# Kernel tuning notes

Measured on AMD Instinct MI355X. Metric: run time of the kernel, lower is better.

Reference implementation:

```python
import jax, jax.numpy as jnp
import numpy as np
import math

B, L, H, D = 4, 2048, 8, 64
FACTOR = 5
SAMPLE_K = min(FACTOR * int(np.ceil(np.log(L))), L)  # U_part = 40
N_TOP = min(FACTOR * int(np.ceil(np.log(L))), L)     # u = 40


def setup_inputs() -> dict:
    key = jax.random.key(0)
    kq, kk, kv, ki = jax.random.split(key, 4)
    queries = jax.random.normal(kq, (B, L, H, D), dtype=jnp.float32)
    keys = jax.random.normal(kk, (B, L, H, D), dtype=jnp.float32)
    values = jax.random.normal(kv, (B, L, H, D), dtype=jnp.float32)
    # ProbSparse random key sampling indices (torch.randint(L_K, (L_Q, sample_k)))
    index_sample = jax.random.randint(ki, (L, SAMPLE_K), 0, L, dtype=jnp.int64)
    return {"queries": queries, "keys": keys, "values": values,
            "index_sample": index_sample}


def reference(queries, keys, values, index_sample):
    # [B, L, H, D] -> [B, H, L, D]
    Q = jnp.transpose(queries, (0, 2, 1, 3))
    K = jnp.transpose(keys, (0, 2, 1, 3))
    V = jnp.transpose(values, (0, 2, 1, 3))
    L_K = K.shape[2]

    # --- _prob_QK ---
    # gather sampled keys per query: [B, H, L_Q, sample_k, D]
    K_sample = K[:, :, index_sample, :]
    # sampled QK dots: [B, H, L_Q, sample_k]
    Q_K_sample = jnp.einsum('bhld,bhlsd->bhls', Q, K_sample)
    # sparsity measurement M = max - mean
    M = Q_K_sample.max(axis=-1) - Q_K_sample.sum(axis=-1) / L_K  # [B, H, L_Q]
    _, M_top = jax.lax.top_k(M, N_TOP)  # [B, H, n_top]
    # gather top queries: [B, H, n_top, D]
    Q_reduce = jnp.take_along_axis(Q, M_top[..., None], axis=2)
    # reduced scores against all keys: [B, H, n_top, L_K]
    scores_top = jnp.einsum('bhud,bhkd->bhuk', Q_reduce, K)

    # --- forward tail ---
    scale = 1.0 / math.sqrt(D)
    attn = jax.nn.softmax(scores_top * scale, axis=-1)  # dropout = identity (eval)
    context = jnp.einsum('bhuk,bhkd->bhud', attn, V)  # [B, H, n_top, D]
    # [B, n_top, H, D]
    return jnp.transpose(context, (0, 2, 1, 3))
```

## Files before the change

### kernel.cpp

```cpp
#include <hip/hip_runtime.h>
#include <hip/hip_bf16.h>

#define BB 4
#define LL 2048
#define HH 8
#define DD 64
#define SK 40
#define NT 40
#define CH 256
#define NCH (LL / CH)
#define QH 20

#define WS 10

typedef float f4 __attribute__((ext_vector_type(4)));

__global__ __launch_bounds__(256, 6) void compute_m_kernel(
        const float* __restrict__ Q, const float* __restrict__ K,
        const int* __restrict__ idx, float* __restrict__ M) {
    __shared__ float2 mlpart[4][HH];

    int blk = blockIdx.x;
    int x = blk & 7, g = blk >> 3;
    int b = x >> 1;
    int l = (g << 1) | (x & 1);
    int t = threadIdx.x;
    int lane = t & 63, w = t >> 6;
    int grp  = lane >> 3;

    const float* Qrow = Q + ((size_t)b * LL + l) * 512 + lane * 8;
    f4 qa = *(const f4*)(Qrow);
    f4 qb = *(const f4*)(Qrow + 4);

    const float* Kb = K + (size_t)b * LL * 512 + lane * 8;
    const int* ib = idx + (size_t)l * SK + w * WS;

    int i0 = ib[0], i1 = ib[1], i2 = ib[2], i3 = ib[3], i4 = ib[4];
    int i5 = ib[5], i6 = ib[6], i7 = ib[7], i8 = ib[8], i9 = ib[9];
    const float* a0 = Kb + (size_t)i0 * 512;
    const float* a1 = Kb + (size_t)i1 * 512;
    const float* a2 = Kb + (size_t)i2 * 512;
    const float* a3 = Kb + (size_t)i3 * 512;
    const float* a4 = Kb + (size_t)i4 * 512;
    const float* a5 = Kb + (size_t)i5 * 512;
    const float* a6 = Kb + (size_t)i6 * 512;
    const float* a7 = Kb + (size_t)i7 * 512;
    const float* a8 = Kb + (size_t)i8 * 512;
    const float* a9 = Kb + (size_t)i9 * 512;

    asm volatile("" : "+v"(qa), "+v"(qb));

    f4 A0, B0, A1, B1, A2, B2, A3, B3, A4, B4;
    f4 A5, B5, A6, B6, A7, B7, A8, B8, A9, B9;

    #define ISSUE(AV, BV, PTR)                                                  \
        asm volatile("global_load_dwordx4 %0, %2, off\n"                        \
                     "global_load_dwordx4 %1, %2, off offset:16"                \
                     : "=&v"(AV), "=&v"(BV) : "v"(PTR))

    float mx = -INFINITY, sm = 0.0f;

    #define CONS(AV, BV, WAIT) do {                                            \
        asm volatile(WAIT : "+v"(AV), "+v"(BV));                               \
        float p = qa.x*AV.x + qa.y*AV.y + qa.z*AV.z + qa.w*AV.w                \
                + qb.x*BV.x + qb.y*BV.y + qb.z*BV.z + qb.w*BV.w;               \
        p += __shfl_xor(p, 1, 64);                                             \
        p += __shfl_xor(p, 2, 64);                                             \
        p += __shfl_xor(p, 4, 64);                                             \
        mx = fmaxf(mx, p);                                                     \
        sm += p;                                                               \
    } while (0)

    ISSUE(A0, B0, a0); ISSUE(A1, B1, a1); ISSUE(A2, B2, a2);
    ISSUE(A3, B3, a3); ISSUE(A4, B4, a4);
    ISSUE(A5, B5, a5); CONS(A0, B0, "s_waitcnt vmcnt(10)");
    ISSUE(A6, B6, a6); CONS(A1, B1, "s_waitcnt vmcnt(10)");
    ISSUE(A7, B7, a7); CONS(A2, B2, "s_waitcnt vmcnt(10)");
    ISSUE(A8, B8, a8); CONS(A3, B3, "s_waitcnt vmcnt(10)");
    ISSUE(A9, B9, a9); CONS(A4, B4, "s_waitcnt vmcnt(10)");
    CONS(A5, B5, "s_waitcnt vmcnt(8)");
    CONS(A6, B6, "s_waitcnt vmcnt(6)");
    CONS(A7, B7, "s_waitcnt vmcnt(4)");
    CONS(A8, B8, "s_waitcnt vmcnt(2)");
    CONS(A9, B9, "s_waitcnt vmcnt(0)");
    #undef ISSUE
    #undef CONS

    if ((lane & 7) == 0)
        mlpart[w][grp] = make_float2(mx, sm);
    __syncthreads();

    if (t < HH) {
        float MX = -INFINITY, SM = 0.0f;
        #pragma unroll
        for (int w2 = 0; w2 < 4; ++w2) {
            float2 ml = mlpart[w2][t];
            MX = fmaxf(MX, ml.x);
            SM += ml.y;
        }
        M[((size_t)b * HH + t) * LL + l] = MX - SM * (1.0f / (float)LL);
    }
}

__global__ __launch_bounds__(256) void topk_kernel(const float* __restrict__ M,
                                                   int* __restrict__ topi) {
    __shared__ unsigned long long keys[LL];
    __shared__ unsigned long long wmax[4];
    __shared__ int win;
    int bh = blockIdx.x;
    int t  = threadIdx.x;
    int lane = t & 63, w = t >> 6;

    unsigned long long kmax = 0ULL;
    #pragma unroll
    for (int j = 0; j < 8; ++j) {
        int i = t + 256 * j;
        unsigned int bits = __float_as_uint(M[(size_t)bh * LL + i]);
        bits = (bits & 0x80000000u) ? ~bits : (bits | 0x80000000u);
        unsigned long long k = ((unsigned long long)bits << 11)
                             | (unsigned int)(LL - 1 - i);
        keys[i] = k;
        if (k > kmax) kmax = k;
    }
    __syncthreads();

    for (int u = 0; u < NT; ++u) {
        unsigned long long k = kmax;
        #pragma unroll
        for (int off = 32; off >= 1; off >>= 1) {
            unsigned long long o = __shfl_xor(k, off, 64);
            if (o > k) k = o;
        }
        if (lane == 0) wmax[w] = k;
        __syncthreads();
        if (t == 0) {
            unsigned long long k0 = wmax[0];
            if (wmax[1] > k0) k0 = wmax[1];
            if (wmax[2] > k0) k0 = wmax[2];
            if (wmax[3] > k0) k0 = wmax[3];
            int i = (LL - 1) - (int)(k0 & 0x7FF);
            topi[bh * NT + u] = i;
            keys[i] = 0ULL;
            win = i;
        }
        __syncthreads();
        if ((win & 255) == t) {
            kmax = 0ULL;
            #pragma unroll
            for (int j = 0; j < 8; ++j) {
                unsigned long long kk = keys[t + 256 * j];
                if (kk > kmax) kmax = kk;
            }
        }
    }
}

__global__ __launch_bounds__(256, 3) void attn_kernel(
        const float* __restrict__ Q, const float* __restrict__ K,
        const float* __restrict__ V, const int* __restrict__ topi,
        float2* __restrict__ pml, float* __restrict__ po) {
    __shared__ float  qs[QH][DD];
    __shared__ float4 e4buf[4][64];
    __shared__ float  oarea[4][QH][DD];
    __shared__ float  mlarea[4][QH][2];

    int blk = blockIdx.x;
    int qh  = blk >> 8;
    int cc2 = blk & 255;
    int c   = cc2 & (NCH - 1);
    int bh  = cc2 >> 3;
    int h = bh & (HH - 1), b = bh >> 3;
    int t = threadIdx.x, lane = t & 63, w = t >> 6;
    int u0 = qh * QH;

    for (int i = t; i < QH * DD; i += 256) {
        int u = i >> 6, d = i & 63;
        int lq = topi[bh * NT + u0 + u];
        qs[u][d] = Q[(((size_t)b * LL + lq) * HH + h) * DD + d];
    }

    int key = c * CH + w * 64 + lane;
    const float4* kr = (const float4*)&K[(((size_t)b * LL + key) * HH + h) * DD];
    float4 kreg[16];
    #pragma unroll
    for (int j = 0; j < 16; ++j) kreg[j] = kr[j];

    float vcol[64];
    const float* vb = &V[(((size_t)b * LL + c * CH + w * 64) * HH + h) * DD + lane];
    #pragma unroll
    for (int j = 0; j < 64; ++j) vcol[j] = vb[(size_t)j * HH * DD];

    __syncthreads();

    for (int uq = 0; uq < QH / 4; ++uq) {
        float o0 = 0, o1 = 0, o2 = 0, o3 = 0;
        float mv0, mv1, mv2, mv3, lv0, lv1, lv2, lv3;
        float4 ev;
        #pragma unroll
        for (int j = 0; j < 4; ++j) {
            int u = uq * 4 + j;
            const float4* q4 = (const float4*)&qs[u][0];
            float s = 0.0f;
            #pragma unroll
            for (int cc = 0; cc < 16; ++cc) {
                float4 qv = q4[cc];
                s += qv.x * kreg[cc].x + qv.y * kreg[cc].y
                   + qv.z * kreg[cc].z + qv.w * kreg[cc].w;
            }
            s *= 0.125f;
            float m = s;
            #pragma unroll
            for (int off = 32; off >= 1; off >>= 1)
                m = fmaxf(m, __shfl_xor(m, off, 64));
            float e = __expf(s - m);
            float ls = e;
            #pragma unroll
            for (int off = 32; off >= 1; off >>= 1)
                ls += __shfl_xor(ls, off, 64);
            if (j == 0) { mv0 = m; lv0 = ls; ev.x = e; }
            if (j == 1) { mv1 = m; lv1 = ls; ev.y = e; }
            if (j == 2) { mv2 = m; lv2 = ls; ev.z = e; }
            if (j == 3) { mv3 = m; lv3 = ls; ev.w = e; }
        }
        e4buf[w][lane] = ev;
        asm volatile("s_waitcnt lgkmcnt(0)" ::: "memory");
        #pragma unroll
        for (int l2 = 0; l2 < 64; ++l2) {
            float4 e = e4buf[w][l2];
            float  v = vcol[l2];
            o0 += e.x * v; o1 += e.y * v; o2 += e.z * v; o3 += e.w * v;
        }
        oarea[w][uq * 4 + 0][lane] = o0;
        oarea[w][uq * 4 + 1][lane] = o1;
        oarea[w][uq * 4 + 2][lane] = o2;
        oarea[w][uq * 4 + 3][lane] = o3;
        if (lane == 0) {
            mlarea[w][uq * 4 + 0][0] = mv0; mlarea[w][uq * 4 + 0][1] = lv0;
            mlarea[w][uq * 4 + 1][0] = mv1; mlarea[w][uq * 4 + 1][1] = lv1;
            mlarea[w][uq * 4 + 2][0] = mv2; mlarea[w][uq * 4 + 2][1] = lv2;
            mlarea[w][uq * 4 + 3][0] = mv3; mlarea[w][uq * 4 + 3][1] = lv3;
        }
    }
    __syncthreads();

    for (int i = t; i < QH * DD; i += 256) {
        int u = i >> 6, d = i & 63;
        float m0 = mlarea[0][u][0], m1 = mlarea[1][u][0];
        float m2 = mlarea[2][u][0], m3 = mlarea[3][u][0];
        float mb = fmaxf(fmaxf(m0, m1), fmaxf(m2, m3));
        float s0 = __expf(m0 - mb), s1 = __expf(m1 - mb);
        float s2 = __expf(m2 - mb), s3 = __expf(m3 - mb);
        float ob = oarea[0][u][d] * s0 + oarea[1][u][d] * s1
                 + oarea[2][u][d] * s2 + oarea[3][u][d] * s3;
        int gu = u0 + u;
        po[((size_t)(bh * NT + gu) * NCH + c) * DD + d] = ob;
        if (d == 0) {
            float lb = mlarea[0][u][1] * s0 + mlarea[1][u][1] * s1
                     + mlarea[2][u][1] * s2 + mlarea[3][u][1] * s3;
            pml[(bh * NT + gu) * NCH + c] = make_float2(mb, lb);
        }
    }
}

__global__ __launch_bounds__(256) void merge_kernel(
        const float2* __restrict__ pml, const float* __restrict__ po,
        float* __restrict__ out) {
    int wid  = blockIdx.x * 4 + (threadIdx.x >> 6);
    int lane = threadIdx.x & 63;
    int u  = wid % NT;
    int bh = wid / NT;
    int h = bh & (HH - 1), b = bh >> 3;
    int base = (bh * NT + u) * NCH;

    float m = -INFINITY;
    #pragma unroll
    for (int cc = 0; cc < NCH; ++cc) m = fmaxf(m, pml[base + cc].x);
    float lsum = 0.0f, o = 0.0f;
    #pragma unroll
    for (int cc = 0; cc < NCH; ++cc) {
        float2 ml = pml[base + cc];
        float sc = __expf(ml.x - m);
        lsum += ml.y * sc;
        o    += po[(size_t)(base + cc) * DD + lane] * sc;
    }
    out[(((size_t)b * NT + u) * HH + h) * DD + lane] = o / lsum;
}

extern "C" void kernel_launch(void* const* d_in, const int* in_sizes, int n_in,
                              void* d_out, int out_size, void* d_ws, size_t ws_size,
                              hipStream_t stream) {
    const float* Q   = (const float*)d_in[0];
    const float* K   = (const float*)d_in[1];
    const float* V   = (const float*)d_in[2];
    const int*   idx = (const int*)d_in[3];
    float* out = (float*)d_out;

    char* ws = (char*)d_ws;
    float*  M    = (float*)ws;                        ws += (size_t)BB * HH * LL * sizeof(float);
    int*    topi = (int*)ws;                          ws += (size_t)BB * HH * NT * sizeof(int);
    float2* pml  = (float2*)ws;                       ws += (size_t)BB * HH * NT * NCH * sizeof(float2);
    float*  po   = (float*)ws;

    hipLaunchKernelGGL(compute_m_kernel, dim3(BB * LL), dim3(256), 0, stream,
                       Q, K, idx, M);
    hipLaunchKernelGGL(topk_kernel, dim3(BB * HH), dim3(256), 0, stream, M, topi);
    hipLaunchKernelGGL(attn_kernel, dim3(2 * BB * HH * NCH), dim3(256), 0, stream,
                       Q, K, V, topi, pml, po);
    hipLaunchKernelGGL(merge_kernel, dim3(BB * HH * NT / 4), dim3(256), 0, stream,
                       pml, po, out);
}
```

Measured before the change: 166.6 us.

## Restructure top-k as per-wave register top-40 then single-wave merge

The top-k selection now keeps each wave's 512 keys in registers and has each wave independently extract its local top-40 by repeated wave-wide shuffle max, with no block barriers inside the loop. The 160 candidates are then merged by one wave into the global top-40. This removes the two __syncthreads per iteration and the 2048-entry shared key array, at the cost of more register pressure and redundant per-wave work.

```diff
diff --git a/kernel.cpp b/kernel.cpp
--- a/kernel.cpp
+++ b/kernel.cpp
@@ -104,53 +104,54 @@
 
 __global__ __launch_bounds__(256) void topk_kernel(const float* __restrict__ M,
                                                    int* __restrict__ topi) {
-    __shared__ unsigned long long keys[LL];
-    __shared__ unsigned long long wmax[4];
-    __shared__ int win;
+    __shared__ unsigned long long cand[192];
     int bh = blockIdx.x;
     int t  = threadIdx.x;
     int lane = t & 63, w = t >> 6;
 
-    unsigned long long kmax = 0ULL;
+    unsigned long long kr[8];
     #pragma unroll
     for (int j = 0; j < 8; ++j) {
-        int i = t + 256 * j;
+        int i = w * 512 + j * 64 + lane;
         unsigned int bits = __float_as_uint(M[(size_t)bh * LL + i]);
         bits = (bits & 0x80000000u) ? ~bits : (bits | 0x80000000u);
-        unsigned long long k = ((unsigned long long)bits << 11)
-                             | (unsigned int)(LL - 1 - i);
-        keys[i] = k;
-        if (k > kmax) kmax = k;
+        kr[j] = ((unsigned long long)bits << 11)
+              | (unsigned int)(LL - 1 - i);
+    }
+    if (t < 32) cand[160 + t] = 0ULL;
+
+    for (int u = 0; u < NT; ++u) {
+        unsigned long long m = kr[0];
+        #pragma unroll
+        for (int j = 1; j < 8; ++j) if (kr[j] > m) m = kr[j];
+        #pragma unroll
+        for (int off = 32; off >= 1; off >>= 1) {
+            unsigned long long o = __shfl_xor(m, off, 64);
+            if (o > m) m = o;
+        }
+        if (lane == 0) cand[w * NT + u] = m;
+        #pragma unroll
+        for (int j = 0; j < 8; ++j) if (kr[j] == m) kr[j] = 0ULL;
     }
     __syncthreads();
 
-    for (int u = 0; u < NT; ++u) {
-        unsigned long long k = kmax;
-        #pragma unroll
-        for (int off = 32; off >= 1; off >>= 1) {
-            unsigned long long o = __shfl_xor(k, off, 64);
-            if (o > k) k = o;
-        }
-        if (lane == 0) wmax[w] = k;
-        __syncthreads();
-        if (t == 0) {
-            unsigned long long k0 = wmax[0];
-            if (wmax[1] > k0) k0 = wmax[1];
-            if (wmax[2] > k0) k0 = wmax[2];
-            if (wmax[3] > k0) k0 = wmax[3];
-            int i = (LL - 1) - (int)(k0 & 0x7FF);
-            topi[bh * NT + u] = i;
-            keys[i] = 0ULL;
-            win = i;
-        }
-        __syncthreads();
-        if ((win & 255) == t) {
-            kmax = 0ULL;
+    if (w == 0) {
+        unsigned long long c0 = cand[lane];
+        unsigned long long c1 = cand[64 + lane];
+        unsigned long long c2 = cand[128 + lane];
+        for (int u = 0; u < NT; ++u) {
+            unsigned long long m = c0;
+            if (c1 > m) m = c1;
+            if (c2 > m) m = c2;
             #pragma unroll
-            for (int j = 0; j < 8; ++j) {
-                unsigned long long kk = keys[t + 256 * j];
-                if (kk > kmax) kmax = kk;
+            for (int off = 32; off >= 1; off >>= 1) {
+                unsigned long long o = __shfl_xor(m, off, 64);
+                if (o > m) m = o;
             }
+            if (lane == 0) topi[bh * NT + u] = (LL - 1) - (int)(m & 0x7FF);
+            if (c0 == m) c0 = 0ULL;
+            if (c1 == m) c1 = 0ULL;
+            if (c2 == m) c2 = 0ULL;
         }
     }
 }
```

After: 174.9 us. 1.05x slower.
